# Performance work log

Measured on AMD Instinct MI355X. Metric: run time of the kernel, lower is better.

## Reference

```python
import math
import numpy as np
import jax
import jax.numpy as jnp

B_IN, B_L1, B_L2 = 10, 6, 3
BATCH, NUM_POINTS = 4, 512
F1, F2, F_OUT = 8, 16, 10
NB = BATCH * NUM_POINTS
N_GRID_S2, N_GRID_SO3 = 24, 144


def _lf(n):
    return math.lgamma(n + 1)


def wigner_d(l, beta):
    """Wigner small-d matrices d^l_{m',m}(beta). beta: np [K] -> [K, 2l+1, 2l+1]."""
    beta = np.asarray(beta, dtype=np.float64)
    K = beta.shape[0]
    d = np.zeros((K, 2 * l + 1, 2 * l + 1))
    c, s = np.cos(beta / 2.0), np.sin(beta / 2.0)
    for mi, mp in enumerate(range(-l, l + 1)):
        for ni, m in enumerate(range(-l, l + 1)):
            k0, k1 = max(0, m - mp), min(l + m, l - mp)
            acc = np.zeros(K)
            for k in range(k0, k1 + 1):
                lg = 0.5 * (_lf(l + mp) + _lf(l - mp) + _lf(l + m) + _lf(l - m)) - _lf(l + m - k) - _lf(k) - _lf(mp - m + k) - _lf(l - mp - k)
                acc = acc + ((-1.0) ** (mp - m + k)) * np.exp(lg) * c ** (2 * l - 2 * k + m - mp) * s ** (mp - m + 2 * k)
            d[:, mi, ni] = acc
    return d


def quad_beta_weights(b):
    """Driscoll-Healy quadrature betas and weights at bandwidth b."""
    k = np.arange(2 * b)
    beta = np.pi * (2 * k + 1) / (4 * b)
    j = np.arange(b)[:, None]
    w = (2.0 / b) * np.sin(beta) * np.sum(np.sin((2 * j + 1) * beta[None, :]) / (2 * j + 1), axis=0)
    return beta, w


# near-identity kernel grids (as in s2cnn): s2 grid 3 betas x 8 alphas, so3 grid x 6 gammas
_b = np.arange(1, 4) * (np.pi / 8) / 3
_a = np.linspace(0, 2 * np.pi, 8, endpoint=False)
_GB1, _GA1 = [g.ravel() for g in np.meshgrid(_b, _a, indexing='ij')]
_g = np.linspace(0, 2 * np.pi, 6, endpoint=False)
_GB2, _GA2, _GG2 = [g.ravel() for g in np.meshgrid(_b, _a, _g, indexing='ij')]

_BETA_IN, _W_IN = quad_beta_weights(B_IN)
_BETA_L1, _W_L1 = quad_beta_weights(B_L1)
_BETA_L2, _W_L2 = quad_beta_weights(B_L2)

# S2 FFT tables: quadrature-weighted d^l_{m,0}(beta_k), l < b_l1
_S2FFT_D = [jnp.asarray((wigner_d(l, _BETA_IN)[:, :, l] * _W_IN[:, None]).astype(np.complex64)) for l in range(B_L1)]
# S2 kernel basis psi1[l]: [24, 2l+1] = d^l_{m,0}(beta_g) e^{-i m alpha_g}
_PSI1 = []
for l in range(B_L1):
    m = np.arange(-l, l + 1)
    _PSI1.append(jnp.asarray((wigner_d(l, _GB1)[:, :, l] * np.exp(-1j * m[None, :] * _GA1[:, None])).astype(np.complex64)))
# SO3 inverse-FFT d matrices at b_l1 quadrature betas
_D_L1 = [jnp.asarray(wigner_d(l, _BETA_L1).astype(np.complex64)) for l in range(B_L1)]
# SO3 FFT tables at b_l1 (output bandwidth b_l2)
_SO3FFT_D = [jnp.asarray((wigner_d(l, _BETA_L1) * _W_L1[:, None, None]).astype(np.complex64)) for l in range(B_L2)]
# SO3 kernel basis psi2[l]: [144, 2l+1, 2l+1] = e^{-i m a} d^l_{mn}(b) e^{-i n g}
_PSI2 = []
for l in range(B_L2):
    m = np.arange(-l, l + 1)
    ph = np.exp(-1j * m[None, :, None] * _GA2[:, None, None]) * np.exp(-1j * m[None, None, :] * _GG2[:, None, None])
    _PSI2.append(jnp.asarray((wigner_d(l, _GB2) * ph).astype(np.complex64)))
_D_L2 = [jnp.asarray(wigner_d(l, _BETA_L2).astype(np.complex64)) for l in range(B_L2)]
_W_INT = jnp.asarray(_W_L2.astype(np.float32))


def s2_fft(x, b_out):
    # x: [n, f, 2b(beta), 2b(alpha)] real -> list_l of [n, f, 2l+1] complex
    two_b = x.shape[-1]
    F = jnp.fft.fft(x, axis=-1)
    out = []
    for l in range(b_out):
        idx = np.arange(-l, l + 1) % two_b
        out.append(jnp.einsum('nfkm,km->nfm', F[..., idx], _S2FFT_D[l]))
    return out


def so3_ifft_list(z, b_out, d_list):
    # z[l]: [n, fo, 2l+1(m), 2l+1(p)] -> real [n, fo, 2b(beta), 2b(alpha), 2b(gamma)]
    n2 = 2 * b_out
    n, fo = z[0].shape[:2]
    Fh = jnp.zeros((n, fo, n2, n2, n2), jnp.complex64)
    for l in range(b_out):
        idx = np.arange(-l, l + 1) % n2
        blk = (2 * l + 1) * jnp.einsum('nomp,kmp->nokmp', z[l], d_list[l])
        Fh = Fh.at[:, :, :, idx[:, None], idx[None, :]].add(blk)
    return jnp.real(jnp.fft.ifft2(Fh, axes=(-2, -1)) * (n2 * n2))


def s2_conv(x, w, bias):
    xs = s2_fft(x, B_L1)
    wc = w.astype(jnp.complex64)
    z = []
    for l in range(B_L1):
        y = jnp.einsum('iog,gm->iom', wc, _PSI1[l])  # kernel spectrum [fi, fo, 2l+1]
        z.append(jnp.einsum('nim,iop->nomp', xs[l], jnp.conj(y)))
    return so3_ifft_list(z, B_L1, _D_L1) + bias[None, :, None, None, None]


def so3_fft(x, b_out):
    # x: [n, f, 2b(beta), 2b(alpha), 2b(gamma)] -> list_l of [n, f, 2l+1, 2l+1]
    two_b = x.shape[-1]
    F = jnp.fft.fft2(x, axes=(-2, -1))
    out = []
    for l in range(b_out):
        idx = np.arange(-l, l + 1) % two_b
        out.append(jnp.einsum('nfkmp,kmp->nfmp', F[:, :, :, idx[:, None], idx[None, :]], _SO3FFT_D[l]))
    return out


def so3_conv(x, w, bias):
    xs = so3_fft(x, B_L2)
    wc = w.astype(jnp.complex64)
    z = []
    for l in range(B_L2):
        y = jnp.einsum('iog,gmp->iomp', wc, _PSI2[l])  # [fi, fo, 2l+1, 2l+1]
        z.append(jnp.einsum('nimk,iopk->nomp', xs[l], jnp.conj(y)))
    return so3_ifft_list(z, B_L2, _D_L2) + bias[None, :, None, None, None]


def so3_integrate(x):
    # mean over alpha, gamma; quadrature-weighted sum over beta
    return jnp.einsum('nfk,k->nf', x.mean(axis=(-2, -1)), _W_INT)


def forward(x, w1, b1, w2, b2, w_out, bias_out):
    h = jax.nn.relu(s2_conv(x, w1, b1))
    h = jax.nn.relu(so3_conv(h, w2, b2))
    feat = so3_integrate(h).reshape(BATCH, NUM_POINTS, F2).transpose(0, 2, 1)  # [B, F2, P]
    pooled = feat.max(axis=-1)  # MaxPool1d(kernel_size=num_points) + squeeze
    return pooled @ w_out.T + bias_out


def setup_inputs():
    ks = jax.random.split(jax.random.key(0), 4)
    return {
        'x': jax.random.normal(ks[0], (NB, 1, 2 * B_IN, 2 * B_IN), jnp.float32),
        'w1': jax.random.normal(ks[1], (1, F1, N_GRID_S2), jnp.float32) * 0.1,
        'b1': jnp.zeros((F1,), jnp.float32),
        'w2': jax.random.normal(ks[2], (F1, F2, N_GRID_SO3), jnp.float32) * 0.05,
        'b2': jnp.zeros((F2,), jnp.float32),
        'w_out': jax.random.normal(ks[3], (F_OUT, F2), jnp.float32) * 0.1,
        'bias_out': jnp.zeros((F_OUT,), jnp.float32),
    }


def reference(x, w1, b1, w2, b2, w_out, bias_out):
    return forward(x, w1, b1, w2, b2, w_out, bias_out)
```

## Files before the change

### kernel.cpp

```cpp
#include <hip/hip_runtime.h>
#include <cmath>

typedef float2 c32;

__device__ __forceinline__ void cmadd(c32& acc, c32 a, float cr, float ci){
    acc.x += a.x*cr - a.y*ci;
    acc.y += a.x*ci + a.y*cr;
}

__host__ __device__ constexpr int M12(int x){ return ((x%12)+12)%12; }
__host__ __device__ constexpr int M6(int x){ return ((x%6)+6)%6; }

#define SQ32 0.86602540378443864676f
#define RT22 0.70710678118654752440f
static constexpr float CW12[12] = {1.f, SQ32, 0.5f, 0.f, -0.5f, -SQ32, -1.f, -SQ32, -0.5f, 0.f, 0.5f, SQ32};
static constexpr float SW12[12] = {0.f, 0.5f, SQ32, 1.f, SQ32, 0.5f, 0.f, -0.5f, -SQ32, -1.f, -SQ32, -0.5f};
static constexpr float CW6[6] = {1.f, 0.5f, -0.5f, -1.f, -0.5f, 0.5f};
static constexpr float SW6[6] = {0.f, SQ32, SQ32, 0.f, -SQ32, -SQ32};
static constexpr float CW8[8] = {1.f, RT22, 0.f, -RT22, -1.f, -RT22, 0.f, RT22};
static constexpr float SW8[8] = {0.f, RT22, 1.f, RT22, 0.f, -RT22, -1.f, -RT22};
static constexpr float CW20_[6] = {1.f, 0.95105651629515357212f, 0.80901699437494742410f,
                                   0.58778525229247312917f, 0.30901699437494742410f, 0.f};
static constexpr float SW20_[6] = {0.f, 0.30901699437494742410f, 0.58778525229247312917f,
                                   0.80901699437494742410f, 0.95105651629515357212f, 1.f};

#define O_CY1  0
#define O_CY2P 528
#define O_XS   (O_CY2P + 14080)
#define O_XS2P (O_XS + 73728)
#define N_C32_TOTAL (O_XS2P + 2048*8*30)

#define O_S2D  0
#define O_D1S  1752
#define O_DG   (O_D1S + 6336)
#define O_D2P  (O_DG + 360)
#define O_FEAT (O_D2P + 360)
#define O_POOL (O_FEAT + 32768)

#define DPI 3.14159265358979323846

__device__ __forceinline__ void cell_decode(int c, int& L, int& m, int& p){
    int base;
    if (c < 1){ L=0; base=0; } else if (c < 6){ L=1; base=1; }
    else if (c < 15){ L=2; base=6; } else if (c < 28){ L=3; base=15; }
    else if (c < 45){ L=4; base=28; } else { L=5; base=45; }
    int r = c - base;
    if (r < 2*L){ m = r>>1; p = (r&1)? L : -L; }
    else { m = L; p = (r - 2*L) - L; }
}

static constexpr double FCT[13] = {1.,1.,2.,6.,24.,120.,720.,5040.,40320.,
                                   362880.,3628800.,39916800.,479001600.};

__device__ __forceinline__ double dipow(double b, int e){
    double r = 1.0;
    while (e){ if (e & 1) r *= b; b *= b; e >>= 1; }
    return r;
}

__device__ double dev_wig(int l, int mp, int m, double beta){
    int k0 = max(0, m - mp), k1 = min(l + m, l - mp);
    double c = cos(0.5*beta), s = sin(0.5*beta);
    double fnum = sqrt(FCT[l+mp]*FCT[l-mp]*FCT[l+m]*FCT[l-m]);
    double acc = 0.0;
    for (int k = k0; k <= k1; ++k){
        double t = fnum / (FCT[l+m-k]*FCT[k]*FCT[mp-m+k]*FCT[l-mp-k])
                 * dipow(c, 2*l-2*k+m-mp) * dipow(s, mp-m+2*k);
        acc += ((mp-m+k) & 1) ? -t : t;
    }
    return acc;
}

__device__ double dev_qw(int b, double beta){
    double s = 0.0;
    for (int j = 0; j < b; ++j) s += sin((2.0*j+1.0)*beta)/(2.0*j+1.0);
    return (2.0/b)*sin(beta)*s;
}

__global__ __launch_bounds__(256) void k_setup(c32* cb, float* fb,
                                               const float* __restrict__ w1,
                                               const float* __restrict__ w2){
    __shared__ float wsh[144];
    __shared__ float s_d2sg[225];
    __shared__ c32 W1s[3][8][5];
    __shared__ c32 Rs[3][5][5];
    int bid = blockIdx.x, tid = threadIdx.x;
    if (bid < 128){
        int o = bid >> 3, i = bid & 7;
        for (int c = tid; c < 144; c += 256) wsh[c] = w2[(i*16+o)*144 + c];
        for (int c = tid; c < 225; c += 256){
            int qi = c%5; int t = c/5; int pi = t%5; t /= 5; int ib = t%3; int l = t/3;
            float v = 0.f;
            if (pi < 2*l+1 && qi < 2*l+1){ double beta = (ib+1)*DPI/24.0; v = (float)dev_wig(l, pi-l, qi-l, beta); }
            s_d2sg[c] = v;
        }
        __syncthreads();
        for (int c = tid; c < 120; c += 256){
            int ib = c/40, r = c%40, ia = r/5, qi = r%5;
            int q = qi - 2; int qm = ((q%6)+6)%6;
            float wr = CW6[qm], wi = SW6[qm];
            float er = 1.f, ei = 0.f, sx = 0.f, sy = 0.f;
            const float* wrow = wsh + ib*48 + ia*6;
            #pragma unroll
            for (int ig = 0; ig < 6; ++ig){
                float w = wrow[ig];
                sx += w*er; sy += w*ei;
                float nr = er*wr - ei*wi; ei = er*wi + ei*wr; er = nr;
            }
            W1s[ib][ia][qi] = make_float2(sx, sy);
        }
        __syncthreads();
        for (int c = tid; c < 75; c += 256){
            int ib = c/25, r = c%25, pi = r/5, qi = r%5;
            int p = pi - 2; int pm = ((p%8)+8)%8;
            float wr = CW8[pm], wi = SW8[pm];
            float er = 1.f, ei = 0.f;
            c32 acc = make_float2(0.f,0.f);
            #pragma unroll
            for (int ia = 0; ia < 8; ++ia){
                c32 wv = W1s[ib][ia][qi];
                acc.x += wv.x*er - wv.y*ei;
                acc.y += wv.x*ei + wv.y*er;
                float nr = er*wr - ei*wi; ei = er*wi + ei*wr; er = nr;
            }
            Rs[ib][pi][qi] = acc;
        }
        __syncthreads();
        for (int c = tid; c < 110; c += 256){
            int cell = c/5, qt = c%5;
            int l, p;
            if (cell == 0){ l=0; p=0; }
            else if (cell < 7){ l=1; p=(cell-1)%3 - 1; }
            else { l=2; p=(cell-7)%5 - 2; }
            c32 acc = make_float2(0.f,0.f);
            if (qt < 2*l+1){
                int q = qt - l;
                #pragma unroll
                for (int ib = 0; ib < 3; ++ib){
                    float d = s_d2sg[(l*3+ib)*25 + (p+l)*5 + (q+l)];
                    c32 rv = Rs[ib][p+2][q+2];
                    acc.x += d*rv.x; acc.y += d*rv.y;
                }
            }
            cb[O_CY2P + ((o*22+cell)*8 + i)*5 + qt] = acc;
        }
        return;
    }
    int gid = (bid-128)*256 + tid;
    if (gid < 1320){
        int mi = gid%11; int t = gid/11; int k = t%20; int l = t/20;
        float v = 0.f;
        if (mi < 2*l+1){
            double beta = DPI*(2*k+1)/40.0;
            v = (float)(dev_wig(l, mi-l, 0, beta) * dev_qw(10, beta));
        }
        fb[O_S2D+gid] = v; return;
    }
    gid -= 1320;
    if (gid < 528){
        int pi = gid%11; int t = gid/11; int l = t%6; int o = t/6;
        c32 acc = make_float2(0.f,0.f);
        if (pi < 2*l+1){
            int p = pi - l;
            int pm = ((p%8)+8)%8;
            float wr = CW8[pm], wi = SW8[pm];
            for (int ib = 0; ib < 3; ++ib){
                float d = (float)dev_wig(l, pi-l, 0, (ib+1)*DPI/24.0);
                float er = 1.f, ei = 0.f, sx = 0.f, sy = 0.f;
                #pragma unroll
                for (int ia = 0; ia < 8; ++ia){
                    float w = w1[o*24 + ib*8 + ia];
                    sx += w*er; sy += w*ei;
                    float nr = er*wr - ei*wi; ei = er*wi + ei*wr; er = nr;
                }
                acc.x += d*sx; acc.y += d*sy;
            }
        }
        cb[O_CY1 + (o*6+l)*11 + pi] = acc;
        return;
    }
    gid -= 528;
    if (gid < 6336){
        int k = gid%12; int t = gid/12; int l = t%8; int cell = t/8;
        int L, m, p; cell_decode(cell, L, m, p);
        float v = 0.f;
        if (l < 6 && l >= L){
            double beta = DPI*(2*k+1)/24.0;
            v = (float)dev_wig(l, m, p, beta);
        }
        fb[O_D1S+gid] = v; return;
    }
    gid -= 6336;
    if (gid < 360){
        int k = gid%12; int slot = gid/12;
        int lm = slot/5, qt = slot%5;
        int l = lm==0?0:(lm<3?1:2);
        int m = lm==0?0:(lm<3?lm-1:lm-3);
        float v = 0.f;
        if (qt < 2*l+1){
            double beta = DPI*(2*k+1)/24.0;
            v = (float)(dev_wig(l, m, qt-l, beta) * dev_qw(6, beta));
        }
        fb[O_DG+gid] = v; return;
    }
    gid -= 360;
    if (gid < 360){
        int lp = gid%4; int t = gid/4; int k = t%6; int cell = t/6;
        int m = cell/5, pi = cell%5, p = pi-2, ap = p<0?-p:p;
        float v = 0.f;
        if (lp < 3 && lp >= m && lp >= ap){
            double beta = DPI*(2*k+1)/12.0;
            v = (float)dev_wig(lp, m, p, beta);
        }
        fb[O_D2P+gid] = v; return;
    }
}

__global__ __launch_bounds__(256) void k_s2fft(const float* __restrict__ x, const float* __restrict__ fb,
                                               c32* __restrict__ XS){
    __shared__ float xsh[1600];
    __shared__ c32 F1[4][20][6];
    int n0 = blockIdx.x*4, tid = threadIdx.x;
    for (int i = tid; i < 1600; i += 256) xsh[i] = x[n0*400 + i];
    __syncthreads();
    for (int i = tid; i < 480; i += 256){
        int nl = i/120, r = i - nl*120, k = r/6, m = r - k*6;
        float wr = CW20_[m], wi = -SW20_[m];
        float er = 1.f, ei = 0.f, ax = 0.f, ay = 0.f;
        const float* row = xsh + nl*400 + k*20;
        #pragma unroll
        for (int a = 0; a < 20; ++a){
            float v = row[a];
            ax += v*er; ay += v*ei;
            float nr = er*wr - ei*wi; ei = er*wi + ei*wr; er = nr;
        }
        F1[nl][k][m] = make_float2(ax, ay);
    }
    __syncthreads();
    if (tid < 144){
        int nl = tid/36, t = tid - nl*36;
        int l = 0; while ((l+1)*(l+1) <= t) ++l;
        int mi = t - l*l; int m = mi - l;
        c32 acc = make_float2(0.f,0.f);
        for (int k = 0; k < 20; ++k){
            float d = fb[O_S2D + (l*20+k)*11 + mi];
            c32 F = (m >= 0) ? F1[nl][k][m] : make_float2(F1[nl][k][-m].x, -F1[nl][k][-m].y);
            acc.x += d*F.x; acc.y += d*F.y;
        }
        XS[(n0+nl)*36 + t] = acc;
    }
}

__global__ __launch_bounds__(256) void k_layer1(const c32* __restrict__ cb, const float* __restrict__ fb,
                                                const float* __restrict__ b1, c32* __restrict__ xs2p){
    __shared__ c32 xs_sh[36];
    __shared__ c32 u1[864];
    __shared__ c32 u2[936];
    __shared__ c32 Gg[432];
    __shared__ c32 Gs[180];
    int tid = threadIdx.x;
    int n = blockIdx.x >> 3, o = blockIdx.x & 7;
    float bias = b1[o];
    if (tid < 36) xs_sh[tid] = cb[O_XS + n*36 + tid];
    __syncthreads();

    for (int c = tid; c < 396; c += 256){
        int l = c/66, mp = c - l*66, m = mp/11, pi = mp - m*11;
        int p = pi - 5, ap = p < 0 ? -p : p;
        c32 v = make_float2(0.f, 0.f);
        if (m <= l && ap <= l){
            c32 a = xs_sh[l*l + l + m];
            c32 b = cb[O_CY1 + o*66 + l*11 + p + l];
            float f = (float)(2*l+1);
            v.x = f*(a.x*b.x - a.y*b.y); v.y = f*(a.x*b.y + a.y*b.x);
        }
        u1[c] = v;
    }
    __syncthreads();

    if (tid < 132){
        int cell = tid >> 1, kh = tid & 1;
        int L, m, p; cell_decode(cell, L, m, p);
        int mp = m*11 + p + 5;
        c32 acc[6];
        #pragma unroll
        for (int j = 0; j < 6; ++j) acc[j] = make_float2(0.f,0.f);
        for (int l = L; l < 6; ++l){
            c32 z = u1[l*66 + mp];
            const float* dp = fb + O_D1S + (cell*8 + l)*12 + kh*6;
            #pragma unroll
            for (int j = 0; j < 6; ++j){
                float d = dp[j];
                acc[j].x += d*z.x; acc[j].y += d*z.y;
            }
        }
        #pragma unroll
        for (int j = 0; j < 6; ++j) u2[mp*12 + kh*6 + j] = acc[j];
    }
    __syncthreads();

    if (tid < 72){
        int m = tid/12, k = tid - m*12;
        c32 S0 = u2[(m*11+5)*12 + k];
        c32 E[5], O[5];
        #pragma unroll
        for (int p = 1; p <= 5; ++p){
            c32 a = u2[(m*11+5+p)*12 + k], b = u2[(m*11+5-p)*12 + k];
            E[p-1] = make_float2(a.x+b.x, a.y+b.y);
            O[p-1] = make_float2(a.x-b.x, a.y-b.y);
        }
        #pragma unroll
        for (int g = 0; g < 6; ++g){
            float vex=0.f, vey=0.f, vox=0.f, voy=0.f;
            #pragma unroll
            for (int p = 1; p <= 5; ++p){
                const float cc = CW12[M12(p*g)], ss = SW12[M12(p*g)];
                float vx = E[p-1].x*cc - O[p-1].y*ss;
                float vy = E[p-1].y*cc + O[p-1].x*ss;
                if (p & 1){ vox += vx; voy += vy; } else { vex += vx; vey += vy; }
            }
            float tex = S0.x + vex, tey = S0.y + vey;
            u1[(m*12+g)*12 + k]   = make_float2(tex + vox, tey + voy);
            u1[(m*12+g+6)*12 + k] = make_float2(tex - vox, tey - voy);
        }
    }
    __syncthreads();

    float* hh = (float*)u2;
    if (tid < 144){
        int g = tid/12, k = tid - g*12;
        c32 t1 = u1[(1*12+g)*12+k], t2 = u1[(2*12+g)*12+k], t3 = u1[(3*12+g)*12+k];
        c32 t4 = u1[(4*12+g)*12+k], t5 = u1[(5*12+g)*12+k];
        float base = u1[(0*12+g)*12+k].x + bias;
        #pragma unroll
        for (int a = 0; a < 6; ++a){
            float od = t1.x*CW12[M12(1*a)] - t1.y*SW12[M12(1*a)]
                     + t3.x*CW12[M12(3*a)] - t3.y*SW12[M12(3*a)]
                     + t5.x*CW12[M12(5*a)] - t5.y*SW12[M12(5*a)];
            float ev = t2.x*CW12[M12(2*a)] - t2.y*SW12[M12(2*a)]
                     + t4.x*CW12[M12(4*a)] - t4.y*SW12[M12(4*a)];
            float h0 = base + 2.f*(ev+od);
            float h1 = base + 2.f*(ev-od);
            hh[(g*12+a)*13+k]     = h0 > 0.f ? h0 : 0.f;
            hh[(g*12+a+6)*13+k]   = h1 > 0.f ? h1 : 0.f;
        }
    }
    __syncthreads();

    if (tid < 144){
        int a = tid/12, k = tid - a*12;
        float hv[12];
        #pragma unroll
        for (int g = 0; g < 12; ++g) hv[g] = hh[(g*12+a)*13+k];
        float s0 = 0.f;
        #pragma unroll
        for (int g = 0; g < 12; ++g) s0 += hv[g];
        Gg[a*12+k] = make_float2(s0, 0.f);
        #pragma unroll
        for (int mg = 1; mg < 3; ++mg){
            float ax = 0.f, ay = 0.f;
            #pragma unroll
            for (int g = 0; g < 12; ++g){
                const int tt = M12(mg*g);
                ax += hv[g]*CW12[tt]; ay -= hv[g]*SW12[tt];
            }
            Gg[(mg*12+a)*12+k] = make_float2(ax, ay);
        }
    }
    __syncthreads();

    if (tid < 108){
        int j = tid/36, rr = tid - j*36, mg = rr/12, k = rr - mg*12;
        const c32* gp = Gg + mg*144 + k;
        if (j == 0){
            float sx = 0.f, sy = 0.f;
            #pragma unroll
            for (int a = 0; a < 6; ++a){
                c32 xa = gp[a*12], ya = gp[(a+6)*12];
                sx += xa.x + ya.x; sy += xa.y + ya.y;
            }
            Gs[(2*3+mg)*12+k] = make_float2(sx, sy);
        } else if (j == 1){
            float Cx=0.f,Cy=0.f,Sx=0.f,Sy=0.f;
            #pragma unroll
            for (int a = 0; a < 6; ++a){
                c32 xa = gp[a*12], ya = gp[(a+6)*12];
                float ux = xa.x - ya.x, uy = xa.y - ya.y;
                const float cc = CW12[a], ss = SW12[a];
                Cx += ux*cc; Cy += uy*cc;
                Sx += ux*ss; Sy += uy*ss;
            }
            Gs[(3*3+mg)*12+k] = make_float2(Cx + Sy, Cy - Sx);
            Gs[(1*3+mg)*12+k] = make_float2(Cx - Sy, Cy + Sx);
        } else {
            float Cx=0.f,Cy=0.f,Sx=0.f,Sy=0.f;
            #pragma unroll
            for (int a = 0; a < 6; ++a){
                c32 xa = gp[a*12], ya = gp[(a+6)*12];
                float ux = xa.x + ya.x, uy = xa.y + ya.y;
                const float cc = CW12[M12(2*a)], ss = SW12[M12(2*a)];
                Cx += ux*cc; Cy += uy*cc;
                Sx += ux*ss; Sy += uy*ss;
            }
            Gs[(4*3+mg)*12+k] = make_float2(Cx + Sy, Cy - Sx);
            Gs[(0*3+mg)*12+k] = make_float2(Cx - Sy, Cy + Sx);
        }
    }
    __syncthreads();

    if (tid < 30){
        int lm = tid/5, qt = tid - lm*5;
        int l = lm==0?0:(lm<3?1:2);
        int m = lm==0?0:(lm<3?lm-1:lm-3);
        c32 acc = make_float2(0.f,0.f);
        if (qt < 2*l+1){
            int q = qt - l;
            #pragma unroll
            for (int k = 0; k < 12; ++k){
                float d = fb[O_DG + tid*12 + k];
                c32 gvv;
                if (q >= 0) gvv = Gs[((m+2)*3 + q)*12 + k];
                else { c32 w = Gs[((2-m)*3 + (-q))*12 + k]; gvv = make_float2(w.x, -w.y); }
                acc.x += d*gvv.x; acc.y += d*gvv.y;
            }
        }
        xs2p[(n*8+o)*30 + tid] = acc;
    }
}

__global__ __launch_bounds__(256) void k_layer2(const c32* __restrict__ cb, const float* __restrict__ fb,
                                                const float* __restrict__ b2, float* __restrict__ feat){
    __shared__ c32 xs2sh[960];
    __shared__ c32 zp2[4][384];
    __shared__ c32 T2[1728];
    __shared__ float part[576];
    __shared__ float wint_sh[6];
    int tid = threadIdx.x, n0 = blockIdx.x*4;
    for (int c = tid; c < 960; c += 256) xs2sh[c] = cb[O_XS2P + n0*240 + c];
    if (tid < 6){ double beta = DPI*(2*tid+1)/12.0; wint_sh[tid] = (float)dev_qw(3, beta); }
    __syncthreads();

    for (int c = tid; c < 352; c += 256){
        int o = c/22, cell = c - o*22;
        int l, lm;
        if (cell == 0){ l=0; lm=0; }
        else if (cell < 7){ l=1; lm=1+(cell-1)/3; }
        else { l=2; lm=3+(cell-7)/5; }
        const c32* cy = cb + O_CY2P + (o*22+cell)*40;
        c32 acc[4];
        #pragma unroll
        for (int nl = 0; nl < 4; ++nl) acc[nl] = make_float2(0.f,0.f);
        #pragma unroll
        for (int i = 0; i < 8; ++i){
            #pragma unroll
            for (int qt = 0; qt < 5; ++qt){
                c32 yv = cy[i*5+qt];
                #pragma unroll
                for (int nl = 0; nl < 4; ++nl){
                    c32 xv = xs2sh[nl*240 + (i*6+lm)*5 + qt];
                    acc[nl].x += xv.x*yv.x - xv.y*yv.y;
                    acc[nl].y += xv.x*yv.y + xv.y*yv.x;
                }
            }
        }
        float f = (float)(2*l+1);
        #pragma unroll
        for (int nl = 0; nl < 4; ++nl)
            zp2[nl][o*24+cell] = make_float2(f*acc[nl].x, f*acc[nl].y);
    }
    __syncthreads();

    for (int nl = 0; nl < 4; ++nl){
        for (int c = tid; c < 288; c += 256){
            int o = c/18, r = c - o*18, k = r/3, m = r - k*3;
            c32 s2v[5];
            #pragma unroll
            for (int pi = 0; pi < 5; ++pi){
                const int p = pi-2; const int ap = p<0?-p:p;
                c32 acc = make_float2(0.f,0.f);
                #pragma unroll
                for (int l = 0; l < 3; ++l){
                    if (l >= ap){
                        float d = fb[O_D2P + ((m*5+pi)*6+k)*4 + l];
                        int cell = (l==0) ? 0 : ((l==1) ? 1+m*3+(p+1) : 7+m*5+(p+2));
                        c32 z = zp2[nl][o*24+cell];
                        acc.x += d*z.x; acc.y += d*z.y;
                    }
                }
                s2v[pi] = acc;
            }
            #pragma unroll
            for (int g = 0; g < 6; ++g){
                c32 t = make_float2(0.f,0.f);
                #pragma unroll
                for (int pi = 0; pi < 5; ++pi){
                    const int tt = M6((pi-2)*g);
                    cmadd(t, s2v[pi], CW6[tt], SW6[tt]);
                }
                T2[((o*6+k)*3+m)*6+g] = t;
            }
        }
        __syncthreads();
        for (int c = tid; c < 576; c += 256){
            int o = c/36, r = c - o*36, k = r/6, g = r - k*6;
            c32 t0 = T2[((o*6+k)*3+0)*6+g];
            c32 t1 = T2[((o*6+k)*3+1)*6+g];
            c32 t2 = T2[((o*6+k)*3+2)*6+g];
            float base = t0.x + b2[o];
            float s = 0.f;
            #pragma unroll
            for (int a = 0; a < 6; ++a){
                float h = base + 2.f*(t1.x*CW6[M6(a)]   - t1.y*SW6[M6(a)])
                               + 2.f*(t2.x*CW6[M6(2*a)] - t2.y*SW6[M6(2*a)]);
                s += h > 0.f ? h : 0.f;
            }
            part[c] = s * wint_sh[k];
        }
        __syncthreads();
        if (tid < 16){
            float s = 0.f;
            #pragma unroll
            for (int j = 0; j < 36; ++j) s += part[tid*36+j];
            feat[(n0+nl)*16+tid] = s * (1.f/36.f);
        }
        __syncthreads();
    }
}

__global__ __launch_bounds__(64) void k_pool(const float* __restrict__ feat, float* __restrict__ pool){
    int b = blockIdx.x >> 4, o = blockIdx.x & 15;
    int tid = threadIdx.x;
    float m = -3.4e38f;
    for (int pt = tid; pt < 512; pt += 64)
        m = fmaxf(m, feat[(b*512+pt)*16 + o]);
    for (int off = 32; off; off >>= 1) m = fmaxf(m, __shfl_down(m, off));
    if (tid == 0) pool[b*16 + o] = m;
}

__global__ __launch_bounds__(64) void k_head(const float* __restrict__ pool, const float* __restrict__ w_out,
                                             const float* __restrict__ bias_out, float* __restrict__ out){
    int tid = threadIdx.x;
    if (tid < 40){
        int b = tid/10, j = tid%10;
        float s = bias_out[j];
        for (int o = 0; o < 16; ++o) s += pool[b*16+o]*w_out[j*16+o];
        out[tid] = s;
    }
}

extern "C" void kernel_launch(void* const* d_in, const int* in_sizes, int n_in,
                              void* d_out, int out_size, void* d_ws, size_t ws_size,
                              hipStream_t stream){
    const float* x        = (const float*)d_in[0];
    const float* w1       = (const float*)d_in[1];
    const float* b1       = (const float*)d_in[2];
    const float* w2       = (const float*)d_in[3];
    const float* b2       = (const float*)d_in[4];
    const float* w_out    = (const float*)d_in[5];
    const float* bias_out = (const float*)d_in[6];
    float* out = (float*)d_out;

    c32*   cb = (c32*)d_ws;
    float* fb = (float*)(cb + N_C32_TOTAL);
    float* feat = fb + O_FEAT;
    float* pool = fb + O_POOL;

    k_setup<<<163, 256, 0, stream>>>(cb, fb, w1, w2);
    k_s2fft<<<512, 256, 0, stream>>>(x, fb, cb + O_XS);
    k_layer1<<<2048*8, 256, 0, stream>>>(cb, fb, b1, cb + O_XS2P);
    k_layer2<<<512, 256, 0, stream>>>(cb, fb, b2, feat);
    k_pool<<<64, 64, 0, stream>>>(feat, pool);
    k_head<<<1, 64, 0, stream>>>(pool, w_out, bias_out, out);
}
```

Measured before the change: 172.3 us.

## Fuse S2 FFT, both conv layers and max-pool into one per-point kernel

```diff
diff --git a/kernel.cpp b/kernel.cpp
--- a/kernel.cpp
+++ b/kernel.cpp
@@ -26,16 +26,14 @@
 
 #define O_CY1  0
 #define O_CY2P 528
-#define O_XS   (O_CY2P + 14080)
-#define O_XS2P (O_XS + 73728)
-#define N_C32_TOTAL (O_XS2P + 2048*8*30)
+#define N_C32_TOTAL (O_CY2P + 14080)
 
 #define O_S2D  0
 #define O_D1S  1752
 #define O_DG   (O_D1S + 6336)
 #define O_D2P  (O_DG + 360)
-#define O_FEAT (O_D2P + 360)
-#define O_POOL (O_FEAT + 32768)
+#define O_WINT (O_D2P + 360)
+#define O_POOL (O_WINT + 8)
 
 #define DPI 3.14159265358979323846
 
@@ -85,6 +83,7 @@
     __shared__ c32 W1s[3][8][5];
     __shared__ c32 Rs[3][5][5];
     int bid = blockIdx.x, tid = threadIdx.x;
+    if (bid == 0 && tid < 64) ((unsigned*)(fb + O_POOL))[tid] = 0u;
     if (bid < 128){
         int o = bid >> 3, i = bid & 7;
         for (int c = tid; c < 144; c += 256) wsh[c] = w2[(i*16+o)*144 + c];
@@ -214,331 +213,318 @@
         }
         fb[O_D2P+gid] = v; return;
     }
-}
-
-__global__ __launch_bounds__(256) void k_s2fft(const float* __restrict__ x, const float* __restrict__ fb,
-                                               c32* __restrict__ XS){
-    __shared__ float xsh[1600];
-    __shared__ c32 F1[4][20][6];
-    int n0 = blockIdx.x*4, tid = threadIdx.x;
-    for (int i = tid; i < 1600; i += 256) xsh[i] = x[n0*400 + i];
-    __syncthreads();
-    for (int i = tid; i < 480; i += 256){
-        int nl = i/120, r = i - nl*120, k = r/6, m = r - k*6;
-        float wr = CW20_[m], wi = -SW20_[m];
-        float er = 1.f, ei = 0.f, ax = 0.f, ay = 0.f;
-        const float* row = xsh + nl*400 + k*20;
-        #pragma unroll
-        for (int a = 0; a < 20; ++a){
-            float v = row[a];
-            ax += v*er; ay += v*ei;
-            float nr = er*wr - ei*wi; ei = er*wi + ei*wr; er = nr;
-        }
-        F1[nl][k][m] = make_float2(ax, ay);
-    }
-    __syncthreads();
-    if (tid < 144){
-        int nl = tid/36, t = tid - nl*36;
-        int l = 0; while ((l+1)*(l+1) <= t) ++l;
-        int mi = t - l*l; int m = mi - l;
-        c32 acc = make_float2(0.f,0.f);
-        for (int k = 0; k < 20; ++k){
-            float d = fb[O_S2D + (l*20+k)*11 + mi];
-            c32 F = (m >= 0) ? F1[nl][k][m] : make_float2(F1[nl][k][-m].x, -F1[nl][k][-m].y);
-            acc.x += d*F.x; acc.y += d*F.y;
-        }
-        XS[(n0+nl)*36 + t] = acc;
-    }
-}
-
-__global__ __launch_bounds__(256) void k_layer1(const c32* __restrict__ cb, const float* __restrict__ fb,
-                                                const float* __restrict__ b1, c32* __restrict__ xs2p){
+    gid -= 360;
+    if (gid < 6){
+        double beta = DPI*(2*gid+1)/12.0;
+        fb[O_WINT+gid] = (float)dev_qw(3, beta); return;
+    }
+}
+
+__global__ __launch_bounds__(256) void k_mega(const float* __restrict__ x,
+                                              const c32* __restrict__ cb,
+                                              const float* __restrict__ fb,
+                                              const float* __restrict__ b1,
+                                              const float* __restrict__ b2,
+                                              unsigned* __restrict__ pool){
     __shared__ c32 xs_sh[36];
-    __shared__ c32 u1[864];
-    __shared__ c32 u2[936];
-    __shared__ c32 Gg[432];
-    __shared__ c32 Gs[180];
-    int tid = threadIdx.x;
-    int n = blockIdx.x >> 3, o = blockIdx.x & 7;
-    float bias = b1[o];
-    if (tid < 36) xs_sh[tid] = cb[O_XS + n*36 + tid];
-    __syncthreads();
-
-    for (int c = tid; c < 396; c += 256){
-        int l = c/66, mp = c - l*66, m = mp/11, pi = mp - m*11;
-        int p = pi - 5, ap = p < 0 ? -p : p;
-        c32 v = make_float2(0.f, 0.f);
-        if (m <= l && ap <= l){
-            c32 a = xs_sh[l*l + l + m];
-            c32 b = cb[O_CY1 + o*66 + l*11 + p + l];
-            float f = (float)(2*l+1);
-            v.x = f*(a.x*b.x - a.y*b.y); v.y = f*(a.x*b.y + a.y*b.x);
-        }
-        u1[c] = v;
-    }
-    __syncthreads();
-
-    if (tid < 132){
-        int cell = tid >> 1, kh = tid & 1;
-        int L, m, p; cell_decode(cell, L, m, p);
-        int mp = m*11 + p + 5;
-        c32 acc[6];
-        #pragma unroll
-        for (int j = 0; j < 6; ++j) acc[j] = make_float2(0.f,0.f);
-        for (int l = L; l < 6; ++l){
-            c32 z = u1[l*66 + mp];
-            const float* dp = fb + O_D1S + (cell*8 + l)*12 + kh*6;
-            #pragma unroll
-            for (int j = 0; j < 6; ++j){
-                float d = dp[j];
-                acc[j].x += d*z.x; acc[j].y += d*z.y;
-            }
-        }
-        #pragma unroll
-        for (int j = 0; j < 6; ++j) u2[mp*12 + kh*6 + j] = acc[j];
-    }
-    __syncthreads();
-
-    if (tid < 72){
-        int m = tid/12, k = tid - m*12;
-        c32 S0 = u2[(m*11+5)*12 + k];
-        c32 E[5], O[5];
-        #pragma unroll
-        for (int p = 1; p <= 5; ++p){
-            c32 a = u2[(m*11+5+p)*12 + k], b = u2[(m*11+5-p)*12 + k];
-            E[p-1] = make_float2(a.x+b.x, a.y+b.y);
-            O[p-1] = make_float2(a.x-b.x, a.y-b.y);
-        }
-        #pragma unroll
-        for (int g = 0; g < 6; ++g){
-            float vex=0.f, vey=0.f, vox=0.f, voy=0.f;
+    __shared__ c32 xs2sh[240];
+    __shared__ c32 U[2232];
+    int n = blockIdx.x, tid = threadIdx.x;
+
+    {
+        float* xsh = (float*)U;
+        c32* F1 = U + 200;
+        for (int i = tid; i < 400; i += 256) xsh[i] = x[n*400 + i];
+        __syncthreads();
+        if (tid < 120){
+            int k = tid/6, m = tid - k*6;
+            float wr = CW20_[m], wi = -SW20_[m];
+            float er = 1.f, ei = 0.f, ax = 0.f, ay = 0.f;
+            const float* row = xsh + k*20;
+            #pragma unroll
+            for (int a = 0; a < 20; ++a){
+                float v = row[a];
+                ax += v*er; ay += v*ei;
+                float nr = er*wr - ei*wi; ei = er*wi + ei*wr; er = nr;
+            }
+            F1[k*6+m] = make_float2(ax, ay);
+        }
+        __syncthreads();
+        if (tid < 36){
+            int l = 0; while ((l+1)*(l+1) <= tid) ++l;
+            int mi = tid - l*l; int m = mi - l;
+            c32 acc = make_float2(0.f,0.f);
+            for (int k = 0; k < 20; ++k){
+                float d = fb[O_S2D + (l*20+k)*11 + mi];
+                c32 F = (m >= 0) ? F1[k*6+m] : make_float2(F1[k*6-m].x, -F1[k*6-m].y);
+                acc.x += d*F.x; acc.y += d*F.y;
+            }
+            xs_sh[tid] = acc;
+        }
+        __syncthreads();
+    }
+
+    c32* u1 = U;
+    c32* u2 = U + 864;
+    c32* Gg = U + 1800;
+    c32* Gs = U + 864;
+    float* hh = (float*)(U + 864);
+
+    for (int o = 0; o < 8; ++o){
+        float bias = b1[o];
+
+        for (int c = tid; c < 396; c += 256){
+            int l = c/66, mp = c - l*66, m = mp/11, pi = mp - m*11;
+            int p = pi - 5, ap = p < 0 ? -p : p;
+            c32 v = make_float2(0.f, 0.f);
+            if (m <= l && ap <= l){
+                c32 a = xs_sh[l*l + l + m];
+                c32 b = cb[O_CY1 + o*66 + l*11 + p + l];
+                float f = (float)(2*l+1);
+                v.x = f*(a.x*b.x - a.y*b.y); v.y = f*(a.x*b.y + a.y*b.x);
+            }
+            u1[c] = v;
+        }
+        __syncthreads();
+
+        if (tid < 132){
+            int cell = tid >> 1, kh = tid & 1;
+            int L, m, p; cell_decode(cell, L, m, p);
+            int mp = m*11 + p + 5;
+            c32 acc[6];
+            #pragma unroll
+            for (int j = 0; j < 6; ++j) acc[j] = make_float2(0.f,0.f);
+            for (int l = L; l < 6; ++l){
+                c32 z = u1[l*66 + mp];
+                const float* dp = fb + O_D1S + (cell*8 + l)*12 + kh*6;
+                #pragma unroll
+                for (int j = 0; j < 6; ++j){
+                    float d = dp[j];
+                    acc[j].x += d*z.x; acc[j].y += d*z.y;
+                }
+            }
+            #pragma unroll
+            for (int j = 0; j < 6; ++j) u2[mp*12 + kh*6 + j] = acc[j];
+        }
+        __syncthreads();
+
+        if (tid < 72){
+            int m = tid/12, k = tid - m*12;
+            c32 S0 = u2[(m*11+5)*12 + k];
+            c32 E[5], O[5];
             #pragma unroll
             for (int p = 1; p <= 5; ++p){
-                const float cc = CW12[M12(p*g)], ss = SW12[M12(p*g)];
-                float vx = E[p-1].x*cc - O[p-1].y*ss;
-                float vy = E[p-1].y*cc + O[p-1].x*ss;
-                if (p & 1){ vox += vx; voy += vy; } else { vex += vx; vey += vy; }
-            }
-            float tex = S0.x + vex, tey = S0.y + vey;
-            u1[(m*12+g)*12 + k]   = make_float2(tex + vox, tey + voy);
-            u1[(m*12+g+6)*12 + k] = make_float2(tex - vox, tey - voy);
-        }
-    }
-    __syncthreads();
-
-    float* hh = (float*)u2;
-    if (tid < 144){
-        int g = tid/12, k = tid - g*12;
-        c32 t1 = u1[(1*12+g)*12+k], t2 = u1[(2*12+g)*12+k], t3 = u1[(3*12+g)*12+k];
-        c32 t4 = u1[(4*12+g)*12+k], t5 = u1[(5*12+g)*12+k];
-        float base = u1[(0*12+g)*12+k].x + bias;
-        #pragma unroll
-        for (int a = 0; a < 6; ++a){
-            float od = t1.x*CW12[M12(1*a)] - t1.y*SW12[M12(1*a)]
-                     + t3.x*CW12[M12(3*a)] - t3.y*SW12[M12(3*a)]
-                     + t5.x*CW12[M12(5*a)] - t5.y*SW12[M12(5*a)];
-            float ev = t2.x*CW12[M12(2*a)] - t2.y*SW12[M12(2*a)]
-                     + t4.x*CW12[M12(4*a)] - t4.y*SW12[M12(4*a)];
-            float h0 = base + 2.f*(ev+od);
-            float h1 = base + 2.f*(ev-od);
-            hh[(g*12+a)*13+k]     = h0 > 0.f ? h0 : 0.f;
-            hh[(g*12+a+6)*13+k]   = h1 > 0.f ? h1 : 0.f;
-        }
-    }
-    __syncthreads();
-
-    if (tid < 144){
-        int a = tid/12, k = tid - a*12;
-        float hv[12];
-        #pragma unroll
-        for (int g = 0; g < 12; ++g) hv[g] = hh[(g*12+a)*13+k];
-        float s0 = 0.f;
-        #pragma unroll
-        for (int g = 0; g < 12; ++g) s0 += hv[g];
-        Gg[a*12+k] = make_float2(s0, 0.f);
-        #pragma unroll
-        for (int mg = 1; mg < 3; ++mg){
-            float ax = 0.f, ay = 0.f;
-            #pragma unroll
-            for (int g = 0; g < 12; ++g){
-                const int tt = M12(mg*g);
-                ax += hv[g]*CW12[tt]; ay -= hv[g]*SW12[tt];
-            }
-            Gg[(mg*12+a)*12+k] = make_float2(ax, ay);
-        }
-    }
-    __syncthreads();
-
-    if (tid < 108){
-        int j = tid/36, rr = tid - j*36, mg = rr/12, k = rr - mg*12;
-        const c32* gp = Gg + mg*144 + k;
-        if (j == 0){
-            float sx = 0.f, sy = 0.f;
+                c32 a = u2[(m*11+5+p)*12 + k], b = u2[(m*11+5-p)*12 + k];
+                E[p-1] = make_float2(a.x+b.x, a.y+b.y);
+                O[p-1] = make_float2(a.x-b.x, a.y-b.y);
+            }
+            #pragma unroll
+            for (int g = 0; g < 6; ++g){
+                float vex=0.f, vey=0.f, vox=0.f, voy=0.f;
+                #pragma unroll
+                for (int p = 1; p <= 5; ++p){
+                    const float cc = CW12[M12(p*g)], ss = SW12[M12(p*g)];
+                    float vx = E[p-1].x*cc - O[p-1].y*ss;
+                    float vy = E[p-1].y*cc + O[p-1].x*ss;
+                    if (p & 1){ vox += vx; voy += vy; } else { vex += vx; vey += vy; }
+                }
+                float tex = S0.x + vex, tey = S0.y + vey;
+                u1[(m*12+g)*12 + k]   = make_float2(tex + vox, tey + voy);
+                u1[(m*12+g+6)*12 + k] = make_float2(tex - vox, tey - voy);
+            }
+        }
+        __syncthreads();
+
+        if (tid < 144){
+            int g = tid/12, k = tid - g*12;
+            c32 t1 = u1[(1*12+g)*12+k], t2 = u1[(2*12+g)*12+k], t3 = u1[(3*12+g)*12+k];
+            c32 t4 = u1[(4*12+g)*12+k], t5 = u1[(5*12+g)*12+k];
+            float base = u1[(0*12+g)*12+k].x + bias;
             #pragma unroll
             for (int a = 0; a < 6; ++a){
-                c32 xa = gp[a*12], ya = gp[(a+6)*12];
-                sx += xa.x + ya.x; sy += xa.y + ya.y;
-            }
-            Gs[(2*3+mg)*12+k] = make_float2(sx, sy);
-        } else if (j == 1){
-            float Cx=0.f,Cy=0.f,Sx=0.f,Sy=0.f;
-            #pragma unroll
-            for (int a = 0; a < 6; ++a){
-                c32 xa = gp[a*12], ya = gp[(a+6)*12];
-                float ux = xa.x - ya.x, uy = xa.y - ya.y;
-                const float cc = CW12[a], ss = SW12[a];
-                Cx += ux*cc; Cy += uy*cc;
-                Sx += ux*ss; Sy += uy*ss;
-            }
-            Gs[(3*3+mg)*12+k] = make_float2(Cx + Sy, Cy - Sx);
-            Gs[(1*3+mg)*12+k] = make_float2(Cx - Sy, Cy + Sx);
-        } else {
-            float Cx=0.f,Cy=0.f,Sx=0.f,Sy=0.f;
-            #pragma unroll
-            for (int a = 0; a < 6; ++a){
-                c32 xa = gp[a*12], ya = gp[(a+6)*12];
-                float ux = xa.x + ya.x, uy = xa.y + ya.y;
-                const float cc = CW12[M12(2*a)], ss = SW12[M12(2*a)];
-                Cx += ux*cc; Cy += uy*cc;
-                Sx += ux*ss; Sy += uy*ss;
-            }
-            Gs[(4*3+mg)*12+k] = make_float2(Cx + Sy, Cy - Sx);
-            Gs[(0*3+mg)*12+k] = make_float2(Cx - Sy, Cy + Sx);
-        }
-    }
-    __syncthreads();
-
-    if (tid < 30){
-        int lm = tid/5, qt = tid - lm*5;
-        int l = lm==0?0:(lm<3?1:2);
-        int m = lm==0?0:(lm<3?lm-1:lm-3);
-        c32 acc = make_float2(0.f,0.f);
-        if (qt < 2*l+1){
-            int q = qt - l;
-            #pragma unroll
-            for (int k = 0; k < 12; ++k){
-                float d = fb[O_DG + tid*12 + k];
-                c32 gvv;
-                if (q >= 0) gvv = Gs[((m+2)*3 + q)*12 + k];
-                else { c32 w = Gs[((2-m)*3 + (-q))*12 + k]; gvv = make_float2(w.x, -w.y); }
-                acc.x += d*gvv.x; acc.y += d*gvv.y;
-            }
-        }
-        xs2p[(n*8+o)*30 + tid] = acc;
-    }
-}
-
-__global__ __launch_bounds__(256) void k_layer2(const c32* __restrict__ cb, const float* __restrict__ fb,
-                                                const float* __restrict__ b2, float* __restrict__ feat){
-    __shared__ c32 xs2sh[960];
-    __shared__ c32 zp2[4][384];
-    __shared__ c32 T2[1728];
-    __shared__ float part[576];
-    __shared__ float wint_sh[6];
-    int tid = threadIdx.x, n0 = blockIdx.x*4;
-    for (int c = tid; c < 960; c += 256) xs2sh[c] = cb[O_XS2P + n0*240 + c];
-    if (tid < 6){ double beta = DPI*(2*tid+1)/12.0; wint_sh[tid] = (float)dev_qw(3, beta); }
-    __syncthreads();
+                float od = t1.x*CW12[M12(1*a)] - t1.y*SW12[M12(1*a)]
+                         + t3.x*CW12[M12(3*a)] - t3.y*SW12[M12(3*a)]
+                         + t5.x*CW12[M12(5*a)] - t5.y*SW12[M12(5*a)];
+                float ev = t2.x*CW12[M12(2*a)] - t2.y*SW12[M12(2*a)]
+                         + t4.x*CW12[M12(4*a)] - t4.y*SW12[M12(4*a)];
+                float h0 = base + 2.f*(ev+od);
+                float h1 = base + 2.f*(ev-od);
+                hh[(g*12+a)*13+k]     = h0 > 0.f ? h0 : 0.f;
+                hh[(g*12+a+6)*13+k]   = h1 > 0.f ? h1 : 0.f;
+            }
+        }
+        __syncthreads();
+
+        if (tid < 144){
+            int a = tid/12, k = tid - a*12;
+            float hv[12];
+            #pragma unroll
+            for (int g = 0; g < 12; ++g) hv[g] = hh[(g*12+a)*13+k];
+            float s0 = 0.f;
+            #pragma unroll
+            for (int g = 0; g < 12; ++g) s0 += hv[g];
+            Gg[a*12+k] = make_float2(s0, 0.f);
+            #pragma unroll
+            for (int mg = 1; mg < 3; ++mg){
+                float ax = 0.f, ay = 0.f;
+                #pragma unroll
+                for (int g = 0; g < 12; ++g){
+                    const int tt = M12(mg*g);
+                    ax += hv[g]*CW12[tt]; ay -= hv[g]*SW12[tt];
+                }
+                Gg[(mg*12+a)*12+k] = make_float2(ax, ay);
+            }
+        }
+        __syncthreads();
+
+        if (tid < 108){
+            int j = tid/36, rr = tid - j*36, mg = rr/12, k = rr - mg*12;
+            const c32* gp = Gg + mg*144 + k;
+            if (j == 0){
+                float sx = 0.f, sy = 0.f;
+                #pragma unroll
+                for (int a = 0; a < 6; ++a){
+                    c32 xa = gp[a*12], ya = gp[(a+6)*12];
+                    sx += xa.x + ya.x; sy += xa.y + ya.y;
+                }
+                Gs[(2*3+mg)*12+k] = make_float2(sx, sy);
+            } else if (j == 1){
+                float Cx=0.f,Cy=0.f,Sx=0.f,Sy=0.f;
+                #pragma unroll
+                for (int a = 0; a < 6; ++a){
+                    c32 xa = gp[a*12], ya = gp[(a+6)*12];
+                    float ux = xa.x - ya.x, uy = xa.y - ya.y;
+                    const float cc = CW12[a], ss = SW12[a];
+                    Cx += ux*cc; Cy += uy*cc;
+                    Sx += ux*ss; Sy += uy*ss;
+                }
+                Gs[(3*3+mg)*12+k] = make_float2(Cx + Sy, Cy - Sx);
+                Gs[(1*3+mg)*12+k] = make_float2(Cx - Sy, Cy + Sx);
+            } else {
+                float Cx=0.f,Cy=0.f,Sx=0.f,Sy=0.f;
+                #pragma unroll
+                for (int a = 0; a < 6; ++a){
+                    c32 xa = gp[a*12], ya = gp[(a+6)*12];
+                    float ux = xa.x + ya.x, uy = xa.y + ya.y;
+                    const float cc = CW12[M12(2*a)], ss = SW12[M12(2*a)];
+                    Cx += ux*cc; Cy += uy*cc;
+                    Sx += ux*ss; Sy += uy*ss;
+                }
+                Gs[(4*3+mg)*12+k] = make_float2(Cx + Sy, Cy - Sx);
+                Gs[(0*3+mg)*12+k] = make_float2(Cx - Sy, Cy + Sx);
+            }
+        }
+        __syncthreads();
+
+        if (tid < 30){
+            int lm = tid/5, qt = tid - lm*5;
+            int l = lm==0?0:(lm<3?1:2);
+            int m = lm==0?0:(lm<3?lm-1:lm-3);
+            c32 acc = make_float2(0.f,0.f);
+            if (qt < 2*l+1){
+                int q = qt - l;
+                #pragma unroll
+                for (int k = 0; k < 12; ++k){
+                    float d = fb[O_DG + tid*12 + k];
+                    c32 gvv;
+                    if (q >= 0) gvv = Gs[((m+2)*3 + q)*12 + k];
+                    else { c32 w = Gs[((2-m)*3 + (-q))*12 + k]; gvv = make_float2(w.x, -w.y); }
+                    acc.x += d*gvv.x; acc.y += d*gvv.y;
+                }
+            }
+            xs2sh[o*30 + tid] = acc;
+        }
+        __syncthreads();
+    }
+
+    c32* zp2 = U;
+    c32* T2  = U + 384;
+    float* part = (float*)U;
 
     for (int c = tid; c < 352; c += 256){
-        int o = c/22, cell = c - o*22;
+        int o2 = c/22, cell = c - o2*22;
         int l, lm;
         if (cell == 0){ l=0; lm=0; }
         else if (cell < 7){ l=1; lm=1+(cell-1)/3; }
         else { l=2; lm=3+(cell-7)/5; }
-        const c32* cy = cb + O_CY2P + (o*22+cell)*40;
-        c32 acc[4];
-        #pragma unroll
-        for (int nl = 0; nl < 4; ++nl) acc[nl] = make_float2(0.f,0.f);
+        const c32* cy = cb + O_CY2P + (o2*22+cell)*40;
+        c32 acc = make_float2(0.f,0.f);
         #pragma unroll
         for (int i = 0; i < 8; ++i){
             #pragma unroll
             for (int qt = 0; qt < 5; ++qt){
+                c32 xv = xs2sh[i*30 + lm*5 + qt];
                 c32 yv = cy[i*5+qt];
-                #pragma unroll
-                for (int nl = 0; nl < 4; ++nl){
-                    c32 xv = xs2sh[nl*240 + (i*6+lm)*5 + qt];
-                    acc[nl].x += xv.x*yv.x - xv.y*yv.y;
-                    acc[nl].y += xv.x*yv.y + xv.y*yv.x;
-                }
+                acc.x += xv.x*yv.x - xv.y*yv.y;
+                acc.y += xv.x*yv.y + xv.y*yv.x;
             }
         }
         float f = (float)(2*l+1);
+        zp2[o2*24+cell] = make_float2(f*acc.x, f*acc.y);
+    }
+    __syncthreads();
+
+    for (int c = tid; c < 288; c += 256){
+        int o2 = c/18, r = c - o2*18, k = r/3, m = r - k*3;
+        c32 s2v[5];
         #pragma unroll
-        for (int nl = 0; nl < 4; ++nl)
-            zp2[nl][o*24+cell] = make_float2(f*acc[nl].x, f*acc[nl].y);
+        for (int pi = 0; pi < 5; ++pi){
+            const int p = pi-2; const int ap = p<0?-p:p;
+            c32 acc = make_float2(0.f,0.f);
+            #pragma unroll
+            for (int l = 0; l < 3; ++l){
+                if (l >= ap){
+                    float d = fb[O_D2P + ((m*5+pi)*6+k)*4 + l];
+                    int cell = (l==0) ? 0 : ((l==1) ? 1+m*3+(p+1) : 7+m*5+(p+2));
+                    c32 z = zp2[o2*24+cell];
+                    acc.x += d*z.x; acc.y += d*z.y;
+                }
+            }
+            s2v[pi] = acc;
+        }
+        #pragma unroll
+        for (int g = 0; g < 6; ++g){
+            c32 t = make_float2(0.f,0.f);
+            #pragma unroll
+            for (int pi = 0; pi < 5; ++pi){
+                const int tt = M6((pi-2)*g);
+                cmadd(t, s2v[pi], CW6[tt], SW6[tt]);
+            }
+            T2[((o2*6+k)*3+m)*6+g] = t;
+        }
     }
     __syncthreads();
 
-    for (int nl = 0; nl < 4; ++nl){
-        for (int c = tid; c < 288; c += 256){
-            int o = c/18, r = c - o*18, k = r/3, m = r - k*3;
-            c32 s2v[5];
-            #pragma unroll
-            for (int pi = 0; pi < 5; ++pi){
-                const int p = pi-2; const int ap = p<0?-p:p;
-                c32 acc = make_float2(0.f,0.f);
-                #pragma unroll
-                for (int l = 0; l < 3; ++l){
-                    if (l >= ap){
-                        float d = fb[O_D2P + ((m*5+pi)*6+k)*4 + l];
-                        int cell = (l==0) ? 0 : ((l==1) ? 1+m*3+(p+1) : 7+m*5+(p+2));
-                        c32 z = zp2[nl][o*24+cell];
-                        acc.x += d*z.x; acc.y += d*z.y;
-                    }
-                }
-                s2v[pi] = acc;
-            }
-            #pragma unroll
-            for (int g = 0; g < 6; ++g){
-                c32 t = make_float2(0.f,0.f);
-                #pragma unroll
-                for (int pi = 0; pi < 5; ++pi){
-                    const int tt = M6((pi-2)*g);
-                    cmadd(t, s2v[pi], CW6[tt], SW6[tt]);
-                }
-                T2[((o*6+k)*3+m)*6+g] = t;
-            }
-        }
-        __syncthreads();
-        for (int c = tid; c < 576; c += 256){
-            int o = c/36, r = c - o*36, k = r/6, g = r - k*6;
-            c32 t0 = T2[((o*6+k)*3+0)*6+g];
-            c32 t1 = T2[((o*6+k)*3+1)*6+g];
-            c32 t2 = T2[((o*6+k)*3+2)*6+g];
-            float base = t0.x + b2[o];
-            float s = 0.f;
-            #pragma unroll
-            for (int a = 0; a < 6; ++a){
-                float h = base + 2.f*(t1.x*CW6[M6(a)]   - t1.y*SW6[M6(a)])
-                               + 2.f*(t2.x*CW6[M6(2*a)] - t2.y*SW6[M6(2*a)]);
-                s += h > 0.f ? h : 0.f;
-            }
-            part[c] = s * wint_sh[k];
-        }
-        __syncthreads();
-        if (tid < 16){
-            float s = 0.f;
-            #pragma unroll
-            for (int j = 0; j < 36; ++j) s += part[tid*36+j];
-            feat[(n0+nl)*16+tid] = s * (1.f/36.f);
-        }
-        __syncthreads();
-    }
-}
-
-__global__ __launch_bounds__(64) void k_pool(const float* __restrict__ feat, float* __restrict__ pool){
-    int b = blockIdx.x >> 4, o = blockIdx.x & 15;
-    int tid = threadIdx.x;
-    float m = -3.4e38f;
-    for (int pt = tid; pt < 512; pt += 64)
-        m = fmaxf(m, feat[(b*512+pt)*16 + o]);
-    for (int off = 32; off; off >>= 1) m = fmaxf(m, __shfl_down(m, off));
-    if (tid == 0) pool[b*16 + o] = m;
-}
-
-__global__ __launch_bounds__(64) void k_head(const float* __restrict__ pool, const float* __restrict__ w_out,
-                                             const float* __restrict__ bias_out, float* __restrict__ out){
+    for (int c = tid; c < 576; c += 256){
+        int o2 = c/36, r = c - o2*36, k = r/6, g = r - k*6;
+        c32 t0 = T2[((o2*6+k)*3+0)*6+g];
+        c32 t1 = T2[((o2*6+k)*3+1)*6+g];
+        c32 t2 = T2[((o2*6+k)*3+2)*6+g];
+        float base = t0.x + b2[o2];
+        float s = 0.f;
+        #pragma unroll
+        for (int a = 0; a < 6; ++a){
+            float h = base + 2.f*(t1.x*CW6[M6(a)]   - t1.y*SW6[M6(a)])
+                           + 2.f*(t2.x*CW6[M6(2*a)] - t2.y*SW6[M6(2*a)]);
+            s += h > 0.f ? h : 0.f;
+        }
+        part[c] = s * fb[O_WINT + k];
+    }
+    __syncthreads();
+
+    if (tid < 16){
+        float s = 0.f;
+        #pragma unroll
+        for (int j = 0; j < 36; ++j) s += part[tid*36+j];
+        float val = s * (1.f/36.f);
+        atomicMax(pool + (n >> 9)*16 + tid, __float_as_uint(val));
+    }
+}
+
+__global__ __launch_bounds__(64) void k_head(const float* __restrict__ pool,
+                                             const float* __restrict__ w_out,
+                                             const float* __restrict__ bias_out,
+                                             float* __restrict__ out){
     int tid = threadIdx.x;
     if (tid < 40){
         int b = tid/10, j = tid%10;
@@ -562,13 +548,8 @@
 
     c32*   cb = (c32*)d_ws;
     float* fb = (float*)(cb + N_C32_TOTAL);
-    float* feat = fb + O_FEAT;
-    float* pool = fb + O_POOL;
 
     k_setup<<<163, 256, 0, stream>>>(cb, fb, w1, w2);
-    k_s2fft<<<512, 256, 0, stream>>>(x, fb, cb + O_XS);
-    k_layer1<<<2048*8, 256, 0, stream>>>(cb, fb, b1, cb + O_XS2P);
-    k_layer2<<<512, 256, 0, stream>>>(cb, fb, b2, feat);
-    k_pool<<<64, 64, 0, stream>>>(feat, pool);
-    k_head<<<1, 64, 0, stream>>>(pool, w_out, bias_out, out);
-}
+    k_mega<<<2048, 256, 0, stream>>>(x, cb, fb, b1, b2, (unsigned*)(fb + O_POOL));
+    k_head<<<1, 64, 0, stream>>>(fb + O_POOL, w_out, bias_out, out);
+}
```

Measured after the change: 206.6 us. 19.9% more time.
